# Performance work log

Measured on AMD Instinct MI355X. Metric: run time of the kernel, lower is better.

The kernel has to match this reference:

```python
import math
import jax, jax.numpy as jnp
import numpy as np

B, Q, M = 4, 512, 8192
LOC_D, SENS_D, EMB_D = 8, 256, 512


def setup_inputs() -> dict:
    key = jax.random.key(0)
    ks = jax.random.split(key, 6)
    location = jax.random.normal(ks[0], (B, Q, LOC_D), dtype=jnp.float32)
    # sds must be positive (they are squared and logged); keep them away from 0
    location_sd = jax.random.uniform(ks[1], (B, Q, LOC_D), dtype=jnp.float32) * 0.9 + 0.1
    memory_locations = jax.random.normal(ks[2], (B, M, LOC_D), dtype=jnp.float32)
    memory_location_sds = jax.random.uniform(ks[3], (B, M, LOC_D), dtype=jnp.float32) * 0.9 + 0.1
    memory_senses = jax.random.normal(ks[4], (B, M, EMB_D), dtype=jnp.float32)
    # sensory_read_proj: Linear(embed_dim -> sensory_dim, bias=False)
    W_read = jax.random.normal(ks[5], (SENS_D, EMB_D), dtype=jnp.float32) / math.sqrt(EMB_D)
    return {
        "location": location,
        "location_sd": location_sd,
        "memory_locations": memory_locations,
        "memory_location_sds": memory_location_sds,
        "memory_senses": memory_senses,
        "W_read": W_read,
    }


def reference(location, location_sd, memory_locations, memory_location_sds, memory_senses, W_read):
    # BidirectionalMemory.read with match_threshold=None, detach_* True (stop_gradient)
    mem_loc = jax.lax.stop_gradient(memory_locations)
    mem_sd = jax.lax.stop_gradient(memory_location_sds)
    mem_sense = jax.lax.stop_gradient(memory_senses)

    # (B,Q,1,D) - (B,1,M,D) -> (B,Q,M,D)
    delta = location[:, :, None, :] - mem_loc[:, None, :, :]
    var = location_sd[:, :, None, :] ** 2 + mem_sd[:, None, :, :] ** 2
    d = delta.shape[-1]
    # -0.5 * sum((delta^2 / (var+eps))^2) - 0.5*log(2pi)*D - sum(log(var))
    log_aff = (
        -0.5 * jnp.sum((delta ** 2 / (var + 1e-8)) ** 2, axis=-1)
        - 0.5 * math.log(2.0 * math.pi) * d
        - jnp.sum(jnp.log(var), axis=-1)
    )  # (B,Q,M)
    weights = jax.nn.softmax(log_aff, axis=-1)  # (B,Q,M)
    pre_sense = jnp.einsum("bqm,bme->bqe", weights, mem_sense)  # (B,Q,EMB_D)
    sense = jnp.einsum("bqe,se->bqs", pre_sense, W_read)  # (B,Q,SENS_D)
    return sense
```

## Files before the change

kernel.cpp:

```cpp
#include <hip/hip_runtime.h>
#include <hip/hip_bf16.h>

#define BB 4
#define QQ 512
#define MM 8192
#define DD 8
#define EE 512
#define SS 256

using f32x4  = __attribute__((ext_vector_type(4))) float;
using bf16x8 = __attribute__((ext_vector_type(8))) short;

static __device__ __forceinline__ unsigned short f2bf(float f) {
  union { __hip_bfloat16 h; unsigned short u; } v;
  v.h = __float2bfloat16(f);
  return v.u;
}

#define QT 2
#define K1_T 512
#define K1_I (MM / K1_T)

__global__ __launch_bounds__(512) void k_aff(
    const float* __restrict__ loc, const float* __restrict__ locsd,
    const float* __restrict__ mloc, const float* __restrict__ msd,
    unsigned short* __restrict__ wts, float* __restrict__ inv)
{
  __shared__ float la_s[QT * K1_I * K1_T];
  __shared__ float red[QT][8];

  const int blk = blockIdx.x;
  const int b   = blk / (QQ / QT);
  const int q0  = (blk % (QQ / QT)) * QT;
  const int t   = threadIdx.x;
  const int lane = t & 63;
  const int wv   = t >> 6;

  float lx[QT][DD], ls2[QT][DD];
#pragma unroll
  for (int qi = 0; qi < QT; ++qi)
#pragma unroll
    for (int d = 0; d < DD; ++d) {
      const int base = ((b * QQ) + q0 + qi) * DD + d;
      lx[qi][d] = loc[base];
      float s = locsd[base];
      ls2[qi][d] = __builtin_fmaf(s, s, 1e-8f);
    }

  const float4* ml4 = reinterpret_cast<const float4*>(mloc + (size_t)b * MM * DD);
  const float4* ms4 = reinterpret_cast<const float4*>(msd  + (size_t)b * MM * DD);

  float mn[QT] = {3.4e38f, 3.4e38f};

#pragma unroll
  for (int i = 0; i < K1_I; ++i) {
    const int m = i * K1_T + t;
    float4 a0 = ml4[2 * m], a1 = ml4[2 * m + 1];
    float4 s0 = ms4[2 * m], s1 = ms4[2 * m + 1];
    float mlv[DD] = {a0.x, a0.y, a0.z, a0.w, a1.x, a1.y, a1.z, a1.w};
    float msv[DD] = {s0.x, s0.y, s0.z, s0.w, s1.x, s1.y, s1.z, s1.w};
    float ms2[DD];
#pragma unroll
    for (int d = 0; d < DD; ++d) ms2[d] = msv[d] * msv[d];
#pragma unroll
    for (int qi = 0; qi < QT; ++qi) {
      float ssum = 0.f, p = 1.f;
#pragma unroll
      for (int d = 0; d < DD; ++d) {
        float v  = ls2[qi][d] + ms2[d];
        float r  = __builtin_amdgcn_rcpf(v);
        float dl = lx[qi][d] - mlv[d];
        float d2 = dl * dl;
        float tt = d2 * r;
        ssum = __builtin_fmaf(tt, tt, ssum);
        p *= v;
      }
      float lavp = __builtin_fmaf(ssum, 0.72134752f, __builtin_amdgcn_logf(p));
      mn[qi] = fminf(mn[qi], lavp);
      la_s[(qi * K1_I + i) * K1_T + t] = lavp;
    }
  }

#pragma unroll
  for (int qi = 0; qi < QT; ++qi)
#pragma unroll
    for (int off = 32; off; off >>= 1)
      mn[qi] = fminf(mn[qi], __shfl_xor(mn[qi], off, 64));
  if (lane == 0) { red[0][wv] = mn[0]; red[1][wv] = mn[1]; }
  __syncthreads();
  float mnb[QT];
#pragma unroll
  for (int qi = 0; qi < QT; ++qi) {
    float m2 = red[qi][0];
#pragma unroll
    for (int w = 1; w < 8; ++w) m2 = fminf(m2, red[qi][w]);
    mnb[qi] = m2;
  }
  __syncthreads();

  float sm[QT] = {0.f, 0.f};
#pragma unroll
  for (int i = 0; i < K1_I; ++i) {
    const int m = i * K1_T + t;
#pragma unroll
    for (int qi = 0; qi < QT; ++qi) {
      float lv = la_s[(qi * K1_I + i) * K1_T + t];
      float e  = __builtin_amdgcn_exp2f(mnb[qi] - lv);
      sm[qi] += e;
      wts[((size_t)(b * QQ + q0 + qi)) * MM + m] = f2bf(e);
    }
  }
#pragma unroll
  for (int qi = 0; qi < QT; ++qi)
#pragma unroll
    for (int off = 32; off; off >>= 1)
      sm[qi] += __shfl_xor(sm[qi], off, 64);
  if (lane == 0) { red[0][wv] = sm[0]; red[1][wv] = sm[1]; }
  __syncthreads();
  if (t == 0) {
#pragma unroll
    for (int qi = 0; qi < QT; ++qi) {
      float s = 0.f;
#pragma unroll
      for (int w = 0; w < 8; ++w) s += red[qi][w];
      inv[b * QQ + q0 + qi] = 1.0f / s;
    }
  }
}

__global__ __launch_bounds__(256) void k_proj(
    const float* __restrict__ V, const float* __restrict__ W,
    unsigned short* __restrict__ projT)
{
  const int m0 = blockIdx.x * 128;
  const int s0 = blockIdx.y * 128;
  const int b  = blockIdx.z;
  const int t = threadIdx.x, lane = t & 63, wv = t >> 6;
  const int wr = wv >> 1, wc = wv & 1;

  __shared__ short lA[128 * 64];
  __shared__ short lB[128 * 64];

  f32x4 acc[4][4] = {};

  const float* Wp = W + (size_t)s0 * EE;
  const float* Vp = V + (size_t)b * MM * EE + (size_t)m0 * EE;

  const int r0 = t >> 4;
  const int c0 = (t & 15) * 4;
  const int swz = (r0 & 7) << 3;

  float4 ra[8], rb[8];

#define P_LOADS(K0)                                                        \
  _Pragma("unroll")                                                        \
  for (int j = 0; j < 8; ++j) {                                            \
    const int row = j * 16 + r0;                                           \
    ra[j] = *reinterpret_cast<const float4*>(&Wp[(size_t)row * EE + (K0) + c0]); \
    rb[j] = *reinterpret_cast<const float4*>(&Vp[(size_t)row * EE + (K0) + c0]); \
  }

  P_LOADS(0)

  for (int ki = 0; ki < 8; ++ki) {
    __syncthreads();
#pragma unroll
    for (int j = 0; j < 8; ++j) {
      const int row = j * 16 + r0;
      const int idx = (row * 64 + c0) ^ swz;
      ushort4 da, db;
      da.x = f2bf(ra[j].x); da.y = f2bf(ra[j].y); da.z = f2bf(ra[j].z); da.w = f2bf(ra[j].w);
      db.x = f2bf(rb[j].x); db.y = f2bf(rb[j].y); db.z = f2bf(rb[j].z); db.w = f2bf(rb[j].w);
      *reinterpret_cast<ushort4*>(&lA[idx]) = da;
      *reinterpret_cast<ushort4*>(&lB[idx]) = db;
    }
    if (ki < 7) { P_LOADS((ki + 1) * 64) }
    __syncthreads();

#pragma unroll
    for (int kk = 0; kk < 2; ++kk) {
      const int kofs = kk * 32 + (lane >> 4) * 8;
      const int r15 = lane & 15;
      bf16x8 af[4], bfv[4];
#pragma unroll
      for (int mi = 0; mi < 4; ++mi) {
        int row = wr * 64 + mi * 16 + r15;
        af[mi] = *reinterpret_cast<const bf16x8*>(&lA[(row * 64 + kofs) ^ ((row & 7) << 3)]);
      }
#pragma unroll
      for (int ni = 0; ni < 4; ++ni) {
        int row = wc * 64 + ni * 16 + r15;
        bfv[ni] = *reinterpret_cast<const bf16x8*>(&lB[(row * 64 + kofs) ^ ((row & 7) << 3)]);
      }
#pragma unroll
      for (int mi = 0; mi < 4; ++mi)
#pragma unroll
        for (int ni = 0; ni < 4; ++ni)
          acc[mi][ni] = __builtin_amdgcn_mfma_f32_16x16x32_bf16(af[mi], bfv[ni], acc[mi][ni], 0, 0, 0);
    }
  }
#undef P_LOADS

  unsigned short* outp = projT + (size_t)b * SS * MM;
  const int fr = (lane >> 4) * 4;
  const int fc = lane & 15;
#pragma unroll
  for (int mi = 0; mi < 4; ++mi)
#pragma unroll
    for (int ni = 0; ni < 4; ++ni)
#pragma unroll
      for (int r = 0; r < 4; ++r) {
        int s = s0 + wr * 64 + mi * 16 + fr + r;
        int m = m0 + wc * 64 + ni * 16 + fc;
        outp[(size_t)s * MM + m] = f2bf(acc[mi][ni][r]);
      }
}

#define KSPLIT 16

__global__ __launch_bounds__(256) void k_wgemm(
    const unsigned short* __restrict__ wts,
    const unsigned short* __restrict__ projT,
    const float* __restrict__ inv,
    float* __restrict__ out)
{
  const int tile = blockIdx.x;
  const int ks   = blockIdx.y;
  const int b    = blockIdx.z;
  const int q0 = (tile >> 1) * 128;
  const int s0 = (tile & 1) * 128;
  const int kbeg = ks * (MM / KSPLIT);
  const int t = threadIdx.x, lane = t & 63, wv = t >> 6;
  const int wr = wv >> 1, wc = wv & 1;

  __shared__ short lA[128 * 64];
  __shared__ short lB[128 * 64];

  f32x4 acc[4][4] = {};
  const unsigned short* A  = wts   + (size_t)b * QQ * MM + (size_t)q0 * MM;
  const unsigned short* Bp = projT + (size_t)b * SS * MM + (size_t)s0 * MM;

  const int r0 = t >> 3;
  const int c0 = (t & 7) * 8;
  const int swz = (r0 & 7) << 3;

  uint4 ua[4], ub[4];

#define G_LOADS(K0)                                                         \
  _Pragma("unroll")                                                         \
  for (int j = 0; j < 4; ++j) {                                             \
    const int row = j * 32 + r0;                                            \
    ua[j] = *reinterpret_cast<const uint4*>(&A[(size_t)row * MM + (K0) + c0]);  \
    ub[j] = *reinterpret_cast<const uint4*>(&Bp[(size_t)row * MM + (K0) + c0]); \
  }

  G_LOADS(kbeg)

  for (int ki = 0; ki < 8; ++ki) {
    __syncthreads();
#pragma unroll
    for (int j = 0; j < 4; ++j) {
      const int row = j * 32 + r0;
      const int idx = (row * 64 + c0) ^ swz;
      *reinterpret_cast<uint4*>(&lA[idx]) = ua[j];
      *reinterpret_cast<uint4*>(&lB[idx]) = ub[j];
    }
    if (ki < 7) { G_LOADS(kbeg + (ki + 1) * 64) }
    __syncthreads();

#pragma unroll
    for (int kk = 0; kk < 2; ++kk) {
      const int kofs = kk * 32 + (lane >> 4) * 8;
      const int r15 = lane & 15;
      bf16x8 af[4], bfv[4];
#pragma unroll
      for (int mi = 0; mi < 4; ++mi) {
        int row = wr * 64 + mi * 16 + r15;
        af[mi] = *reinterpret_cast<const bf16x8*>(&lA[(row * 64 + kofs) ^ ((row & 7) << 3)]);
      }
#pragma unroll
      for (int ni = 0; ni < 4; ++ni) {
        int row = wc * 64 + ni * 16 + r15;
        bfv[ni] = *reinterpret_cast<const bf16x8*>(&lB[(row * 64 + kofs) ^ ((row & 7) << 3)]);
      }
#pragma unroll
      for (int mi = 0; mi < 4; ++mi)
#pragma unroll
        for (int ni = 0; ni < 4; ++ni)
          acc[mi][ni] = __builtin_amdgcn_mfma_f32_16x16x32_bf16(af[mi], bfv[ni], acc[mi][ni], 0, 0, 0);
    }
  }
#undef G_LOADS

  const int fr = (lane >> 4) * 4;
  const int fc = lane & 15;
  const float* invb = inv + b * QQ;
#pragma unroll
  for (int mi = 0; mi < 4; ++mi)
#pragma unroll
    for (int r = 0; r < 4; ++r) {
      const int q = q0 + wr * 64 + mi * 16 + fr + r;
      const float iv = invb[q];
#pragma unroll
      for (int ni = 0; ni < 4; ++ni) {
        const int s = s0 + wc * 64 + ni * 16 + fc;
        atomicAdd(&out[(size_t)(b * QQ + q) * SS + s], acc[mi][ni][r] * iv);
      }
    }
}


extern "C" void kernel_launch(void* const* d_in, const int* in_sizes, int n_in,
                              void* d_out, int out_size, void* d_ws, size_t ws_size,
                              hipStream_t stream) {
  const float* loc    = (const float*)d_in[0];
  const float* locsd  = (const float*)d_in[1];
  const float* mloc   = (const float*)d_in[2];
  const float* msd    = (const float*)d_in[3];
  const float* msense = (const float*)d_in[4];
  const float* wread  = (const float*)d_in[5];
  float* out = (float*)d_out;

  const size_t wts_bytes  = (size_t)BB * QQ * MM * 2;
  const size_t proj_bytes = (size_t)BB * SS * MM * 2;
  const size_t inv_bytes  = (size_t)BB * QQ * 4;
  if (ws_size < wts_bytes + proj_bytes + inv_bytes) return;

  unsigned short* wts   = (unsigned short*)d_ws;
  unsigned short* projT = (unsigned short*)((char*)d_ws + wts_bytes);
  float*          inv   = (float*)((char*)d_ws + wts_bytes + proj_bytes);

  hipMemsetAsync(d_out, 0, (size_t)out_size * sizeof(float), stream);

  hipLaunchKernelGGL(k_aff, dim3(BB * QQ / QT), dim3(K1_T), 0, stream,
                     loc, locsd, mloc, msd, wts, inv);
  hipLaunchKernelGGL(k_proj, dim3(MM / 128, SS / 128, BB), dim3(256), 0, stream,
                     msense, wread, projT);
  hipLaunchKernelGGL(k_wgemm, dim3(8, KSPLIT, BB), dim3(256), 0, stream,
                     wts, projT, inv, out);
}
```

Baseline: 124.4 us.

## Replace split-K atomics with bf16 partial buffers and a separate reduce kernel

```diff
diff --git a/kernel.cpp b/kernel.cpp
--- a/kernel.cpp
+++ b/kernel.cpp
@@ -216,13 +216,13 @@
       }
 }
 
-#define KSPLIT 16
+#define KSPLIT 8
+#define PSLICE ((size_t)BB * QQ * SS)
 
 __global__ __launch_bounds__(256) void k_wgemm(
     const unsigned short* __restrict__ wts,
     const unsigned short* __restrict__ projT,
-    const float* __restrict__ inv,
-    float* __restrict__ out)
+    unsigned short* __restrict__ part)
 {
   const int tile = blockIdx.x;
   const int ks   = blockIdx.y;
@@ -256,7 +256,7 @@
 
   G_LOADS(kbeg)
 
-  for (int ki = 0; ki < 8; ++ki) {
+  for (int ki = 0; ki < 16; ++ki) {
     __syncthreads();
 #pragma unroll
     for (int j = 0; j < 4; ++j) {
@@ -265,7 +265,7 @@
       *reinterpret_cast<uint4*>(&lA[idx]) = ua[j];
       *reinterpret_cast<uint4*>(&lB[idx]) = ub[j];
     }
-    if (ki < 7) { G_LOADS(kbeg + (ki + 1) * 64) }
+    if (ki < 15) { G_LOADS(kbeg + (ki + 1) * 64) }
     __syncthreads();
 
 #pragma unroll
@@ -292,21 +292,44 @@
   }
 #undef G_LOADS
 
+  unsigned short* pp = part + (size_t)ks * PSLICE + (size_t)b * QQ * SS;
   const int fr = (lane >> 4) * 4;
   const int fc = lane & 15;
-  const float* invb = inv + b * QQ;
 #pragma unroll
   for (int mi = 0; mi < 4; ++mi)
 #pragma unroll
     for (int r = 0; r < 4; ++r) {
       const int q = q0 + wr * 64 + mi * 16 + fr + r;
-      const float iv = invb[q];
 #pragma unroll
       for (int ni = 0; ni < 4; ++ni) {
         const int s = s0 + wc * 64 + ni * 16 + fc;
-        atomicAdd(&out[(size_t)(b * QQ + q) * SS + s], acc[mi][ni][r] * iv);
-      }
-    }
+        pp[(size_t)q * SS + s] = f2bf(acc[mi][ni][r]);
+      }
+    }
+}
+
+__global__ __launch_bounds__(256) void k_reduce(
+    const unsigned int* __restrict__ part32,
+    const float* __restrict__ inv,
+    float* __restrict__ out)
+{
+  const int idx = blockIdx.x * 256 + threadIdx.x;
+  const int lin = idx * 2;
+  if (lin >= BB * QQ * SS) return;
+  const int qg = lin / SS;
+  float s0 = 0.f, s1 = 0.f;
+#pragma unroll
+  for (int ks = 0; ks < KSPLIT; ++ks) {
+    unsigned int v = part32[ks * (PSLICE / 2) + idx];
+    union { unsigned int u; float f; } a, c;
+    a.u = (v & 0xffffu) << 16;
+    c.u = v & 0xffff0000u;
+    s0 += a.f;
+    s1 += c.f;
+  }
+  const float iv = inv[qg];
+  float2 o; o.x = s0 * iv; o.y = s1 * iv;
+  *reinterpret_cast<float2*>(&out[lin]) = o;
 }
 
 
@@ -323,19 +346,21 @@
 
   const size_t wts_bytes  = (size_t)BB * QQ * MM * 2;
   const size_t proj_bytes = (size_t)BB * SS * MM * 2;
+  const size_t part_bytes = PSLICE * KSPLIT * 2;
   const size_t inv_bytes  = (size_t)BB * QQ * 4;
-  if (ws_size < wts_bytes + proj_bytes + inv_bytes) return;
+  if (ws_size < wts_bytes + proj_bytes + part_bytes + inv_bytes) return;
 
   unsigned short* wts   = (unsigned short*)d_ws;
   unsigned short* projT = (unsigned short*)((char*)d_ws + wts_bytes);
-  float*          inv   = (float*)((char*)d_ws + wts_bytes + proj_bytes);
-
-  hipMemsetAsync(d_out, 0, (size_t)out_size * sizeof(float), stream);
+  unsigned short* part  = (unsigned short*)((char*)d_ws + wts_bytes + proj_bytes);
+  float*          inv   = (float*)((char*)d_ws + wts_bytes + proj_bytes + part_bytes);
 
   hipLaunchKernelGGL(k_aff, dim3(BB * QQ / QT), dim3(K1_T), 0, stream,
                      loc, locsd, mloc, msd, wts, inv);
   hipLaunchKernelGGL(k_proj, dim3(MM / 128, SS / 128, BB), dim3(256), 0, stream,
                      msense, wread, projT);
   hipLaunchKernelGGL(k_wgemm, dim3(8, KSPLIT, BB), dim3(256), 0, stream,
-                     wts, projT, inv, out);
-}
+                     wts, projT, part);
+  hipLaunchKernelGGL(k_reduce, dim3((BB * QQ * SS / 2 + 255) / 256), dim3(256), 0, stream,
+                     (const unsigned int*)part, inv, out);
+}
```

After: 108.1 us. 1.15x faster.

## Replace atomic split-K accumulation with partial buffers and a separate reduce kernel

Applied to the files above, without the earlier changes.

```diff
diff --git a/kernel.cpp b/kernel.cpp
--- a/kernel.cpp
+++ b/kernel.cpp
@@ -216,20 +216,24 @@
       }
 }
 
-#define KSPLIT 16
+#define PSLICE ((size_t)BB * QQ * SS)
 
 __global__ __launch_bounds__(256) void k_wgemm(
     const unsigned short* __restrict__ wts,
     const unsigned short* __restrict__ projT,
-    const float* __restrict__ inv,
-    float* __restrict__ out)
+    float* __restrict__ part, int ksn, int mslice)
 {
-  const int tile = blockIdx.x;
-  const int ks   = blockIdx.y;
-  const int b    = blockIdx.z;
+  const int nblk8 = ksn * 4;
+  const int hw   = blockIdx.x;
+  const int virt = (hw & 7) * nblk8 + (hw >> 3);
+  const int ks   = virt >> 5;
+  const int tile = virt & 7;
+  const int b    = (virt >> 3) & 3;
+
   const int q0 = (tile >> 1) * 128;
   const int s0 = (tile & 1) * 128;
-  const int kbeg = ks * (MM / KSPLIT);
+  const int kbeg  = ks * mslice;
+  const int niter = mslice >> 6;
   const int t = threadIdx.x, lane = t & 63, wv = t >> 6;
   const int wr = wv >> 1, wc = wv & 1;
 
@@ -256,7 +260,7 @@
 
   G_LOADS(kbeg)
 
-  for (int ki = 0; ki < 8; ++ki) {
+  for (int ki = 0; ki < niter; ++ki) {
     __syncthreads();
 #pragma unroll
     for (int j = 0; j < 4; ++j) {
@@ -265,7 +269,7 @@
       *reinterpret_cast<uint4*>(&lA[idx]) = ua[j];
       *reinterpret_cast<uint4*>(&lB[idx]) = ub[j];
     }
-    if (ki < 7) { G_LOADS(kbeg + (ki + 1) * 64) }
+    if (ki + 1 < niter) { G_LOADS(kbeg + (ki + 1) * 64) }
     __syncthreads();
 
 #pragma unroll
@@ -292,21 +296,46 @@
   }
 #undef G_LOADS
 
-  const int fr = (lane >> 4) * 4;
-  const int fc = lane & 15;
-  const float* invb = inv + b * QQ;
+  float* pp = part + (size_t)ks * PSLICE + (size_t)(tile * 4 + b) * 16384 + (size_t)t * 4;
 #pragma unroll
   for (int mi = 0; mi < 4; ++mi)
 #pragma unroll
-    for (int r = 0; r < 4; ++r) {
-      const int q = q0 + wr * 64 + mi * 16 + fr + r;
-      const float iv = invb[q];
-#pragma unroll
-      for (int ni = 0; ni < 4; ++ni) {
-        const int s = s0 + wc * 64 + ni * 16 + fc;
-        atomicAdd(&out[(size_t)(b * QQ + q) * SS + s], acc[mi][ni][r] * iv);
-      }
-    }
+    for (int ni = 0; ni < 4; ++ni)
+      *reinterpret_cast<float4*>(pp + (size_t)(mi * 4 + ni) * 1024) =
+          *reinterpret_cast<float4*>(&acc[mi][ni]);
+}
+
+__global__ __launch_bounds__(256) void k_reduce(
+    const float4* __restrict__ part4,
+    const float* __restrict__ inv,
+    float* __restrict__ out, int ksn)
+{
+  const int bu = blockIdx.x;
+  const int tile = bu >> 2, b = bu & 3;
+  const int q0 = (tile >> 1) * 128, s0 = (tile & 1) * 128;
+  const int t = threadIdx.x, lane = t & 63, wv = t >> 6;
+  const int wr = wv >> 1, wc = wv & 1;
+  const size_t base4 = (size_t)bu * 4096 + t;
+
+#pragma unroll
+  for (int ci = 0; ci < 2; ++ci) {
+    const int c = blockIdx.y * 2 + ci;
+    const int mi = c >> 2, ni = c & 3;
+    float4 a = {0.f, 0.f, 0.f, 0.f};
+#pragma unroll 4
+    for (int ks = 0; ks < ksn; ++ks) {
+      float4 v = part4[(size_t)ks * (PSLICE / 4) + base4 + (size_t)c * 256];
+      a.x += v.x; a.y += v.y; a.z += v.z; a.w += v.w;
+    }
+    const int qb = q0 + wr * 64 + mi * 16 + (lane >> 4) * 4;
+    const int s  = s0 + wc * 64 + ni * 16 + (lane & 15);
+    float* op = out + (size_t)(b * QQ + qb) * SS + s;
+    const float* ivp = inv + b * QQ + qb;
+    op[0 * SS] = a.x * ivp[0];
+    op[1 * SS] = a.y * ivp[1];
+    op[2 * SS] = a.z * ivp[2];
+    op[3 * SS] = a.w * ivp[3];
+  }
 }
 
 
@@ -324,18 +353,25 @@
   const size_t wts_bytes  = (size_t)BB * QQ * MM * 2;
   const size_t proj_bytes = (size_t)BB * SS * MM * 2;
   const size_t inv_bytes  = (size_t)BB * QQ * 4;
-  if (ws_size < wts_bytes + proj_bytes + inv_bytes) return;
+  const size_t slice_bytes = PSLICE * 4;
+
+  const size_t fixed = wts_bytes + proj_bytes + inv_bytes;
+  if (ws_size < fixed + 4 * slice_bytes) return;
+  int ksn = 4;
+  if (ws_size >= fixed + 16 * slice_bytes) ksn = 16;
+  else if (ws_size >= fixed + 8 * slice_bytes) ksn = 8;
 
   unsigned short* wts   = (unsigned short*)d_ws;
   unsigned short* projT = (unsigned short*)((char*)d_ws + wts_bytes);
   float*          inv   = (float*)((char*)d_ws + wts_bytes + proj_bytes);
-
-  hipMemsetAsync(d_out, 0, (size_t)out_size * sizeof(float), stream);
+  float*          part  = (float*)((char*)d_ws + fixed);
 
   hipLaunchKernelGGL(k_aff, dim3(BB * QQ / QT), dim3(K1_T), 0, stream,
                      loc, locsd, mloc, msd, wts, inv);
   hipLaunchKernelGGL(k_proj, dim3(MM / 128, SS / 128, BB), dim3(256), 0, stream,
                      msense, wread, projT);
-  hipLaunchKernelGGL(k_wgemm, dim3(8, KSPLIT, BB), dim3(256), 0, stream,
-                     wts, projT, inv, out);
-}
+  hipLaunchKernelGGL(k_wgemm, dim3(32 * ksn), dim3(256), 0, stream,
+                     wts, projT, part, ksn, MM / ksn);
+  hipLaunchKernelGGL(k_reduce, dim3(32, 8), dim3(256), 0, stream,
+                     (const float4*)part, inv, out, ksn);
+}
```

After: 112.3 us. -9.7%, faster.

## Fuse affinity softmax with weight GEMM using split-M flash-style partials and merge

Applied to the files above, without the earlier changes.

```diff
diff --git a/kernel.cpp b/kernel.cpp
--- a/kernel.cpp
+++ b/kernel.cpp
@@ -8,6 +8,11 @@
 #define EE 512
 #define SS 256
 
+#define QG 16
+#define MSP 8
+#define MSL (MM / MSP)
+#define NQG (BB * QQ / QG)
+
 using f32x4  = __attribute__((ext_vector_type(4))) float;
 using bf16x8 = __attribute__((ext_vector_type(8))) short;
 
@@ -15,117 +20,6 @@
   union { __hip_bfloat16 h; unsigned short u; } v;
   v.h = __float2bfloat16(f);
   return v.u;
-}
-
-#define QT 2
-#define K1_T 512
-#define K1_I (MM / K1_T)
-
-__global__ __launch_bounds__(512) void k_aff(
-    const float* __restrict__ loc, const float* __restrict__ locsd,
-    const float* __restrict__ mloc, const float* __restrict__ msd,
-    unsigned short* __restrict__ wts, float* __restrict__ inv)
-{
-  __shared__ float la_s[QT * K1_I * K1_T];
-  __shared__ float red[QT][8];
-
-  const int blk = blockIdx.x;
-  const int b   = blk / (QQ / QT);
-  const int q0  = (blk % (QQ / QT)) * QT;
-  const int t   = threadIdx.x;
-  const int lane = t & 63;
-  const int wv   = t >> 6;
-
-  float lx[QT][DD], ls2[QT][DD];
-#pragma unroll
-  for (int qi = 0; qi < QT; ++qi)
-#pragma unroll
-    for (int d = 0; d < DD; ++d) {
-      const int base = ((b * QQ) + q0 + qi) * DD + d;
-      lx[qi][d] = loc[base];
-      float s = locsd[base];
-      ls2[qi][d] = __builtin_fmaf(s, s, 1e-8f);
-    }
-
-  const float4* ml4 = reinterpret_cast<const float4*>(mloc + (size_t)b * MM * DD);
-  const float4* ms4 = reinterpret_cast<const float4*>(msd  + (size_t)b * MM * DD);
-
-  float mn[QT] = {3.4e38f, 3.4e38f};
-
-#pragma unroll
-  for (int i = 0; i < K1_I; ++i) {
-    const int m = i * K1_T + t;
-    float4 a0 = ml4[2 * m], a1 = ml4[2 * m + 1];
-    float4 s0 = ms4[2 * m], s1 = ms4[2 * m + 1];
-    float mlv[DD] = {a0.x, a0.y, a0.z, a0.w, a1.x, a1.y, a1.z, a1.w};
-    float msv[DD] = {s0.x, s0.y, s0.z, s0.w, s1.x, s1.y, s1.z, s1.w};
-    float ms2[DD];
-#pragma unroll
-    for (int d = 0; d < DD; ++d) ms2[d] = msv[d] * msv[d];
-#pragma unroll
-    for (int qi = 0; qi < QT; ++qi) {
-      float ssum = 0.f, p = 1.f;
-#pragma unroll
-      for (int d = 0; d < DD; ++d) {
-        float v  = ls2[qi][d] + ms2[d];
-        float r  = __builtin_amdgcn_rcpf(v);
-        float dl = lx[qi][d] - mlv[d];
-        float d2 = dl * dl;
-        float tt = d2 * r;
-        ssum = __builtin_fmaf(tt, tt, ssum);
-        p *= v;
-      }
-      float lavp = __builtin_fmaf(ssum, 0.72134752f, __builtin_amdgcn_logf(p));
-      mn[qi] = fminf(mn[qi], lavp);
-      la_s[(qi * K1_I + i) * K1_T + t] = lavp;
-    }
-  }
-
-#pragma unroll
-  for (int qi = 0; qi < QT; ++qi)
-#pragma unroll
-    for (int off = 32; off; off >>= 1)
-      mn[qi] = fminf(mn[qi], __shfl_xor(mn[qi], off, 64));
-  if (lane == 0) { red[0][wv] = mn[0]; red[1][wv] = mn[1]; }
-  __syncthreads();
-  float mnb[QT];
-#pragma unroll
-  for (int qi = 0; qi < QT; ++qi) {
-    float m2 = red[qi][0];
-#pragma unroll
-    for (int w = 1; w < 8; ++w) m2 = fminf(m2, red[qi][w]);
-    mnb[qi] = m2;
-  }
-  __syncthreads();
-
-  float sm[QT] = {0.f, 0.f};
-#pragma unroll
-  for (int i = 0; i < K1_I; ++i) {
-    const int m = i * K1_T + t;
-#pragma unroll
-    for (int qi = 0; qi < QT; ++qi) {
-      float lv = la_s[(qi * K1_I + i) * K1_T + t];
-      float e  = __builtin_amdgcn_exp2f(mnb[qi] - lv);
-      sm[qi] += e;
-      wts[((size_t)(b * QQ + q0 + qi)) * MM + m] = f2bf(e);
-    }
-  }
-#pragma unroll
-  for (int qi = 0; qi < QT; ++qi)
-#pragma unroll
-    for (int off = 32; off; off >>= 1)
-      sm[qi] += __shfl_xor(sm[qi], off, 64);
-  if (lane == 0) { red[0][wv] = sm[0]; red[1][wv] = sm[1]; }
-  __syncthreads();
-  if (t == 0) {
-#pragma unroll
-    for (int qi = 0; qi < QT; ++qi) {
-      float s = 0.f;
-#pragma unroll
-      for (int w = 0; w < 8; ++w) s += red[qi][w];
-      inv[b * QQ + q0 + qi] = 1.0f / s;
-    }
-  }
 }
 
 __global__ __launch_bounds__(256) void k_proj(
@@ -216,97 +110,217 @@
       }
 }
 
-#define KSPLIT 16
-
-__global__ __launch_bounds__(256) void k_wgemm(
-    const unsigned short* __restrict__ wts,
+__global__ __launch_bounds__(256, 2) void k_fused(
+    const float* __restrict__ loc, const float* __restrict__ locsd,
+    const float* __restrict__ mloc, const float* __restrict__ msd,
     const unsigned short* __restrict__ projT,
-    const float* __restrict__ inv,
-    float* __restrict__ out)
+    float* __restrict__ opart, float* __restrict__ mn_g,
+    float* __restrict__ sum_g)
 {
-  const int tile = blockIdx.x;
-  const int ks   = blockIdx.y;
-  const int b    = blockIdx.z;
-  const int q0 = (tile >> 1) * 128;
-  const int s0 = (tile & 1) * 128;
-  const int kbeg = ks * (MM / KSPLIT);
+  __shared__ float la_s[8 * MSL];
+  __shared__ unsigned short p_s[QG * MSL];
+  __shared__ float lx_s[QG][DD], ls2_s[QG][DD];
+  __shared__ float red[QG][4];
+
+  const int hw = blockIdx.x;
+  const int ms = hw & 7;
+  const int qg = hw >> 3;
+  const int b  = qg >> 5;
+  const int q0 = (qg & 31) * QG;
   const int t = threadIdx.x, lane = t & 63, wv = t >> 6;
-  const int wr = wv >> 1, wc = wv & 1;
-
-  __shared__ short lA[128 * 64];
-  __shared__ short lB[128 * 64];
-
-  f32x4 acc[4][4] = {};
-  const unsigned short* A  = wts   + (size_t)b * QQ * MM + (size_t)q0 * MM;
-  const unsigned short* Bp = projT + (size_t)b * SS * MM + (size_t)s0 * MM;
-
-  const int r0 = t >> 3;
-  const int c0 = (t & 7) * 8;
-  const int swz = (r0 & 7) << 3;
-
-  uint4 ua[4], ub[4];
-
-#define G_LOADS(K0)                                                         \
+
+  if (t < QG * DD) {
+    const int qq = t >> 3, d = t & 7;
+    const int base = (b * QQ + q0 + qq) * DD + d;
+    lx_s[qq][d] = loc[base];
+    float s = locsd[base];
+    ls2_s[qq][d] = __builtin_fmaf(s, s, 1e-8f);
+  }
+
+  const float4* ml4 = reinterpret_cast<const float4*>(mloc + (size_t)b * MM * DD);
+  const float4* ms4 = reinterpret_cast<const float4*>(msd  + (size_t)b * MM * DD);
+  float mlv[2][2][DD], ms2[2][2][DD];
+#pragma unroll
+  for (int c = 0; c < 2; ++c)
+#pragma unroll
+    for (int p = 0; p < 2; ++p) {
+      const int m = ms * MSL + c * 512 + 2 * t + p;
+      float4 a0 = ml4[2 * m], a1 = ml4[2 * m + 1];
+      float4 s0 = ms4[2 * m], s1 = ms4[2 * m + 1];
+      mlv[c][p][0] = a0.x; mlv[c][p][1] = a0.y; mlv[c][p][2] = a0.z; mlv[c][p][3] = a0.w;
+      mlv[c][p][4] = a1.x; mlv[c][p][5] = a1.y; mlv[c][p][6] = a1.z; mlv[c][p][7] = a1.w;
+      ms2[c][p][0] = s0.x * s0.x; ms2[c][p][1] = s0.y * s0.y;
+      ms2[c][p][2] = s0.z * s0.z; ms2[c][p][3] = s0.w * s0.w;
+      ms2[c][p][4] = s1.x * s1.x; ms2[c][p][5] = s1.y * s1.y;
+      ms2[c][p][6] = s1.z * s1.z; ms2[c][p][7] = s1.w * s1.w;
+    }
+  __syncthreads();
+
+  float rs[QG];
+#pragma unroll
+  for (int q = 0; q < QG; ++q) rs[q] = 0.f;
+
+#pragma unroll
+  for (int sub = 0; sub < 2; ++sub) {
+    float mn8[8];
+#pragma unroll
+    for (int q8 = 0; q8 < 8; ++q8) {
+      const int q = sub * 8 + q8;
+      float lxq[DD], lsq[DD];
+#pragma unroll
+      for (int d = 0; d < DD; d += 4) {
+        float4 v1 = *reinterpret_cast<const float4*>(&lx_s[q][d]);
+        lxq[d] = v1.x; lxq[d + 1] = v1.y; lxq[d + 2] = v1.z; lxq[d + 3] = v1.w;
+        float4 v2 = *reinterpret_cast<const float4*>(&ls2_s[q][d]);
+        lsq[d] = v2.x; lsq[d + 1] = v2.y; lsq[d + 2] = v2.z; lsq[d + 3] = v2.w;
+      }
+      float mnq = 3.4e38f;
+#pragma unroll
+      for (int c = 0; c < 2; ++c) {
+        float la2[2];
+#pragma unroll
+        for (int p = 0; p < 2; ++p) {
+          float ssum = 0.f, pr = 1.f;
+#pragma unroll
+          for (int d = 0; d < DD; ++d) {
+            float v  = lsq[d] + ms2[c][p][d];
+            float r  = __builtin_amdgcn_rcpf(v);
+            float dl = lxq[d] - mlv[c][p][d];
+            float d2 = dl * dl;
+            float tt = d2 * r;
+            ssum = __builtin_fmaf(tt, tt, ssum);
+            pr *= v;
+          }
+          la2[p] = __builtin_fmaf(ssum, 0.72134752f, __builtin_amdgcn_logf(pr));
+          mnq = fminf(mnq, la2[p]);
+        }
+        float2 wr2; wr2.x = la2[0]; wr2.y = la2[1];
+        *reinterpret_cast<float2*>(&la_s[q8 * MSL + c * 512 + 2 * t]) = wr2;
+      }
+      mn8[q8] = mnq;
+    }
+#pragma unroll
+    for (int q8 = 0; q8 < 8; ++q8) {
+      float v = mn8[q8];
+#pragma unroll
+      for (int off = 32; off; off >>= 1) v = fminf(v, __shfl_xor(v, off, 64));
+      if (lane == 0) red[q8][wv] = v;
+    }
+    __syncthreads();
+    float mnb[8];
+#pragma unroll
+    for (int q8 = 0; q8 < 8; ++q8) {
+      mnb[q8] = fminf(fminf(red[q8][0], red[q8][1]), fminf(red[q8][2], red[q8][3]));
+      if (t == q8)
+        mn_g[((size_t)qg * MSP + ms) * QG + sub * 8 + q8] = mnb[q8];
+    }
+    __syncthreads();
+#pragma unroll
+    for (int q8 = 0; q8 < 8; ++q8) {
+      const int q = sub * 8 + q8;
+      const int swz = (q & 7) << 4;
+#pragma unroll
+      for (int c = 0; c < 2; ++c) {
+        float2 la2 = *reinterpret_cast<const float2*>(&la_s[q8 * MSL + c * 512 + 2 * t]);
+        float e0 = __builtin_amdgcn_exp2f(mnb[q8] - la2.x);
+        float e1 = __builtin_amdgcn_exp2f(mnb[q8] - la2.y);
+        rs[q] += e0 + e1;
+        unsigned int pk = (unsigned int)f2bf(e0) | ((unsigned int)f2bf(e1) << 16);
+        *reinterpret_cast<unsigned int*>(
+            (char*)p_s + (((q * MSL + c * 512 + 2 * t) * 2) ^ swz)) = pk;
+      }
+    }
+  }
+
+  __syncthreads();
+#pragma unroll
+  for (int q = 0; q < QG; ++q) {
+    float v = rs[q];
+#pragma unroll
+    for (int off = 32; off; off >>= 1) v += __shfl_xor(v, off, 64);
+    if (lane == 0) red[q][wv] = v;
+  }
+  __syncthreads();
+#pragma unroll
+  for (int q = 0; q < QG; ++q)
+    if (t == q)
+      sum_g[((size_t)qg * MSP + ms) * QG + q] = red[q][0] + red[q][1] + red[q][2] + red[q][3];
+
+  const unsigned short* pTb = projT + (size_t)b * SS * MM + (size_t)ms * MSL;
+  const int s0w = wv * 64;
+  const int qf = lane & 15;
+  const int kf = (lane >> 4) * 8;
+  const int aswz = (qf & 7) << 4;
+  f32x4 acc[4] = {};
+
+#define LDA(CH) (*reinterpret_cast<const bf16x8*>( \
+    (const char*)p_s + (((qf * MSL + (CH) * 32 + kf) * 2) ^ aswz)))
+#define LOADB(U, CH)                                                        \
   _Pragma("unroll")                                                         \
-  for (int j = 0; j < 4; ++j) {                                             \
-    const int row = j * 32 + r0;                                            \
-    ua[j] = *reinterpret_cast<const uint4*>(&A[(size_t)row * MM + (K0) + c0]);  \
-    ub[j] = *reinterpret_cast<const uint4*>(&Bp[(size_t)row * MM + (K0) + c0]); \
-  }
-
-  G_LOADS(kbeg)
-
-  for (int ki = 0; ki < 8; ++ki) {
-    __syncthreads();
-#pragma unroll
-    for (int j = 0; j < 4; ++j) {
-      const int row = j * 32 + r0;
-      const int idx = (row * 64 + c0) ^ swz;
-      *reinterpret_cast<uint4*>(&lA[idx]) = ua[j];
-      *reinterpret_cast<uint4*>(&lB[idx]) = ub[j];
-    }
-    if (ki < 7) { G_LOADS(kbeg + (ki + 1) * 64) }
-    __syncthreads();
-
-#pragma unroll
-    for (int kk = 0; kk < 2; ++kk) {
-      const int kofs = kk * 32 + (lane >> 4) * 8;
-      const int r15 = lane & 15;
-      bf16x8 af[4], bfv[4];
-#pragma unroll
-      for (int mi = 0; mi < 4; ++mi) {
-        int row = wr * 64 + mi * 16 + r15;
-        af[mi] = *reinterpret_cast<const bf16x8*>(&lA[(row * 64 + kofs) ^ ((row & 7) << 3)]);
-      }
-#pragma unroll
-      for (int ni = 0; ni < 4; ++ni) {
-        int row = wc * 64 + ni * 16 + r15;
-        bfv[ni] = *reinterpret_cast<const bf16x8*>(&lB[(row * 64 + kofs) ^ ((row & 7) << 3)]);
-      }
-#pragma unroll
-      for (int mi = 0; mi < 4; ++mi)
-#pragma unroll
-        for (int ni = 0; ni < 4; ++ni)
-          acc[mi][ni] = __builtin_amdgcn_mfma_f32_16x16x32_bf16(af[mi], bfv[ni], acc[mi][ni], 0, 0, 0);
-    }
-  }
-#undef G_LOADS
-
-  const int fr = (lane >> 4) * 4;
-  const int fc = lane & 15;
-  const float* invb = inv + b * QQ;
-#pragma unroll
-  for (int mi = 0; mi < 4; ++mi)
+  for (int ni = 0; ni < 4; ++ni)                                            \
+    U[ni] = *reinterpret_cast<const uint4*>(                                \
+        pTb + (size_t)(s0w + ni * 16 + qf) * MM + (CH) * 32 + kf);
+
+  uint4 u0[4], u1[4];
+  bf16x8 a0, a1;
+  LOADB(u0, 0) a0 = LDA(0);
+#pragma unroll 2
+  for (int ch = 0; ch < 32; ch += 2) {
+    LOADB(u1, ch + 1) a1 = LDA(ch + 1);
+#pragma unroll
+    for (int ni = 0; ni < 4; ++ni)
+      acc[ni] = __builtin_amdgcn_mfma_f32_16x16x32_bf16(
+          a0, *reinterpret_cast<const bf16x8*>(&u0[ni]), acc[ni], 0, 0, 0);
+    if (ch + 2 < 32) { LOADB(u0, ch + 2) a0 = LDA(ch + 2); }
+#pragma unroll
+    for (int ni = 0; ni < 4; ++ni)
+      acc[ni] = __builtin_amdgcn_mfma_f32_16x16x32_bf16(
+          a1, *reinterpret_cast<const bf16x8*>(&u1[ni]), acc[ni], 0, 0, 0);
+  }
+#undef LDA
+#undef LOADB
+
+  float* op = opart + ((size_t)qg * MSP + ms) * (QG * SS);
+#pragma unroll
+  for (int ni = 0; ni < 4; ++ni)
 #pragma unroll
     for (int r = 0; r < 4; ++r) {
-      const int q = q0 + wr * 64 + mi * 16 + fr + r;
-      const float iv = invb[q];
-#pragma unroll
-      for (int ni = 0; ni < 4; ++ni) {
-        const int s = s0 + wc * 64 + ni * 16 + fc;
-        atomicAdd(&out[(size_t)(b * QQ + q) * SS + s], acc[mi][ni][r] * iv);
-      }
-    }
+      const int q = (lane >> 4) * 4 + r;
+      const int s = s0w + ni * 16 + qf;
+      op[q * SS + s] = acc[ni][r];
+    }
+}
+
+__global__ __launch_bounds__(256) void k_merge(
+    const float* __restrict__ opart, const float* __restrict__ mn_g,
+    const float* __restrict__ sum_g, float* __restrict__ out)
+{
+  const int row = blockIdx.x * 4 + (threadIdx.x >> 6);
+  const int lane = threadIdx.x & 63;
+  const int qg = row >> 4, q = row & 15;
+
+  const float* mnp = mn_g  + (size_t)qg * MSP * QG + q;
+  const float* smp = sum_g + (size_t)qg * MSP * QG + q;
+  float mns[MSP], gmn = 3.4e38f;
+#pragma unroll
+  for (int i = 0; i < MSP; ++i) { mns[i] = mnp[i * QG]; gmn = fminf(gmn, mns[i]); }
+  float gsum = 0.f, sc[MSP];
+#pragma unroll
+  for (int i = 0; i < MSP; ++i) {
+    sc[i] = __builtin_amdgcn_exp2f(gmn - mns[i]);
+    gsum = __builtin_fmaf(smp[i * QG], sc[i], gsum);
+  }
+  float o[4] = {0.f, 0.f, 0.f, 0.f};
+  const float* ob = opart + (size_t)qg * MSP * (QG * SS) + q * SS;
+#pragma unroll
+  for (int i = 0; i < MSP; ++i)
+#pragma unroll
+    for (int j = 0; j < 4; ++j)
+      o[j] = __builtin_fmaf(ob[(size_t)i * (QG * SS) + j * 64 + lane], sc[i], o[j]);
+  const float inv = 1.0f / gsum;
+  float* orow = out + (size_t)row * SS;
+#pragma unroll
+  for (int j = 0; j < 4; ++j) orow[j * 64 + lane] = o[j] * inv;
 }
 
 
@@ -321,21 +335,20 @@
   const float* wread  = (const float*)d_in[5];
   float* out = (float*)d_out;
 
-  const size_t wts_bytes  = (size_t)BB * QQ * MM * 2;
-  const size_t proj_bytes = (size_t)BB * SS * MM * 2;
-  const size_t inv_bytes  = (size_t)BB * QQ * 4;
-  if (ws_size < wts_bytes + proj_bytes + inv_bytes) return;
-
-  unsigned short* wts   = (unsigned short*)d_ws;
-  unsigned short* projT = (unsigned short*)((char*)d_ws + wts_bytes);
-  float*          inv   = (float*)((char*)d_ws + wts_bytes + proj_bytes);
-
-  hipMemsetAsync(d_out, 0, (size_t)out_size * sizeof(float), stream);
-
-  hipLaunchKernelGGL(k_aff, dim3(BB * QQ / QT), dim3(K1_T), 0, stream,
-                     loc, locsd, mloc, msd, wts, inv);
+  const size_t proj_bytes  = (size_t)BB * SS * MM * 2;
+  const size_t opart_bytes = (size_t)NQG * MSP * QG * SS * 4;
+  const size_t mn_bytes    = (size_t)NQG * MSP * QG * 4;
+  if (ws_size < proj_bytes + opart_bytes + 2 * mn_bytes) return;
+
+  unsigned short* projT = (unsigned short*)d_ws;
+  float* opart = (float*)((char*)d_ws + proj_bytes);
+  float* mn_g  = (float*)((char*)d_ws + proj_bytes + opart_bytes);
+  float* sum_g = (float*)((char*)d_ws + proj_bytes + opart_bytes + mn_bytes);
+
   hipLaunchKernelGGL(k_proj, dim3(MM / 128, SS / 128, BB), dim3(256), 0, stream,
                      msense, wread, projT);
-  hipLaunchKernelGGL(k_wgemm, dim3(8, KSPLIT, BB), dim3(256), 0, stream,
-                     wts, projT, inv, out);
-}
+  hipLaunchKernelGGL(k_fused, dim3(NQG * MSP), dim3(256), 0, stream,
+                     loc, locsd, mloc, msd, projT, opart, mn_g, sum_g);
+  hipLaunchKernelGGL(k_merge, dim3(BB * QQ / 4), dim3(256), 0, stream,
+                     opart, mn_g, sum_g, out);
+}
```

After: 115.6 us. 1.08x faster.
